# Kernel tuning notes

Measured on AMD Instinct MI355X. Metric: run time of the kernel, lower is better.

Reference implementation:

```python
import jax, jax.numpy as jnp
import numpy as np
from jax import lax

# Mamba2 block (training path: mamba_split_conv1d_scan_combined equivalent)
B = 2; L = 2048; D_MODEL = 2048
INTER = 4096          # ssm_intermediate_size
NH = 64; HD = INTER // NH   # num_heads, head_dim
N = 128               # ssm_state_size
G = 1                 # n_groups
K = 4                 # conv kernel
CS = 256              # chunk size
EPS = 1e-5
CONV_DIM = INTER + 2 * G * N          # 4352
PROJ_DIM = INTER + CONV_DIM + NH      # 8512


def setup_inputs() -> dict:
    key = jax.random.key(0)
    ks = jax.random.split(key, 4)
    std = 0.02
    return {
        "hidden_states": jax.random.normal(ks[0], (B, L, D_MODEL), jnp.float32),
        "W_in": jax.random.normal(ks[1], (PROJ_DIM, D_MODEL), jnp.float32) * std,
        "conv_w": jax.random.normal(ks[2], (CONV_DIM, K), jnp.float32) * std,
        "conv_b": jnp.zeros((CONV_DIM,), jnp.float32),
        "dt_bias": jnp.ones((NH,), jnp.float32),
        "A_log": jnp.log(jnp.arange(1, NH + 1, dtype=jnp.float32)),
        "D": jnp.ones((NH,), jnp.float32),
        "norm_w": jnp.ones((INTER,), jnp.float32),
        "W_out": jax.random.normal(ks[3], (D_MODEL, INTER), jnp.float32) * std,
    }


def _segsum(x):
    # x: [..., s] -> [..., s, s] lower-triangular cumulative sums (masked with -inf)
    s = x.shape[-1]
    xc = jnp.cumsum(x, axis=-1)
    d = xc[..., :, None] - xc[..., None, :]
    return jnp.where(jnp.tril(jnp.ones((s, s), dtype=bool)), d, -jnp.inf)


def _forward(hidden_states, W_in, conv_w, conv_b, dt_bias, A_log, D, norm_w, W_out):
    proj = hidden_states @ W_in.T                              # [B,L,PROJ_DIM]
    gate = proj[..., :INTER]
    hBC = proj[..., INTER:INTER + CONV_DIM]
    dt = proj[..., INTER + CONV_DIM:]                          # [B,L,NH]

    # causal depthwise conv1d + silu
    xc = hBC.transpose(0, 2, 1)                                # [B,CONV_DIM,L]
    y = lax.conv_general_dilated(
        xc, conv_w[:, None, :], (1,), [(K - 1, 0)],
        dimension_numbers=("NCH", "OIH", "NCH"), feature_group_count=CONV_DIM)
    hBC = jax.nn.silu(y + conv_b[None, :, None]).transpose(0, 2, 1)

    x = hBC[..., :INTER].reshape(B, L, NH, HD)
    Bm = hBC[..., INTER:INTER + G * N].reshape(B, L, G, N)
    Cm = hBC[..., INTER + G * N:].reshape(B, L, G, N)

    dtv = jax.nn.softplus(dt + dt_bias)                        # [B,L,NH], dt_softplus=True
    A = -jnp.exp(A_log)                                        # [NH]

    # ---- chunked selective scan (SSD) ----
    c = L // CS
    xch = x.reshape(B, c, CS, NH, HD)
    dtch = dtv.reshape(B, c, CS, NH)
    Bh = jnp.repeat(Bm.reshape(B, c, CS, G, N), NH // G, axis=3)   # [B,c,s,NH,N]
    Ch = jnp.repeat(Cm.reshape(B, c, CS, G, N), NH // G, axis=3)

    dA = (dtch * A).transpose(0, 3, 1, 2)                      # [B,NH,c,s]
    Acum = jnp.cumsum(dA, axis=-1)                             # [B,NH,c,s]
    Lmat = jnp.exp(_segsum(dA))                                # [B,NH,c,s,s]

    # within-chunk (diagonal block) output
    Ydiag = jnp.einsum("bcihn,bcjhn,bhcij,bcjh,bcjhp->bcihp",
                       Ch, Bh, Lmat, dtch, xch)

    # per-chunk states
    decay_states = jnp.exp(Acum[..., -1:] - Acum)              # [B,NH,c,s]
    states = jnp.einsum("bcjhn,bhcj,bcjh,bcjhp->bchpn",
                        Bh, decay_states, dtch, xch)           # [B,c,NH,HD,N]

    # inter-chunk recurrence (scan over chunks)
    chunk_decay = jnp.exp(Acum[..., -1])                       # [B,NH,c]

    def step(carry, inp):
        st, dec = inp
        new = dec[:, :, None, None] * carry + st
        return new, carry                                      # emit state at chunk start

    init = jnp.zeros((B, NH, HD, N), dtype=x.dtype)
    _, prev = lax.scan(step, init,
                       (states.transpose(1, 0, 2, 3, 4), chunk_decay.transpose(2, 0, 1)))
    prev = prev.transpose(1, 0, 2, 3, 4)                       # [B,c,NH,HD,N]

    Yoff = jnp.einsum("bcihn,bchpn,bhci->bcihp", Ch, prev, jnp.exp(Acum))

    Y = (Ydiag + Yoff).reshape(B, L, NH, HD) + x * D[None, None, :, None]
    yout = Y.reshape(B, L, INTER)

    # gated RMSNorm (norm_before_gate=False): gate first, then normalize
    yout = yout * jax.nn.silu(gate)
    yout = yout * lax.rsqrt(jnp.mean(yout * yout, axis=-1, keepdims=True) + EPS) * norm_w
    return yout @ W_out.T                                      # [B,L,D_MODEL]


def reference(hidden_states, W_in, conv_w, conv_b, dt_bias, A_log, D, norm_w, W_out):
    return _forward(hidden_states, W_in, conv_w, conv_b, dt_bias, A_log, D, norm_w, W_out)
```

## Files before the change

kernel.cpp:

```cpp
#include <hip/hip_runtime.h>
#include <cstdint>

typedef __bf16 bf16;
typedef __bf16 bf16x8 __attribute__((ext_vector_type(8)));
typedef __bf16 bf16x4 __attribute__((ext_vector_type(4)));
typedef float  f32x4  __attribute__((ext_vector_type(4)));

#define BQ     2
#define LQ     2048
#define DMODEL 2048
#define INTER  4096
#define NH     64
#define HD     64
#define NS     128
#define CS     256
#define NC     8
#define CONVD  4352
#define PROJD  8512
#define PROJP  8576
#define MTOT   4096
#define EPSF   1e-5f
#define LOG2E  1.44269504088896f

__device__ __forceinline__ void async_ld16(const bf16* g, bf16* l) {
  __builtin_amdgcn_global_load_lds(
      (__attribute__((address_space(1))) void*)(uintptr_t)g,
      (__attribute__((address_space(3))) void*)l, 16, 0, 0);
}

__device__ __forceinline__ float siluf(float x) { return x / (1.f + expf(-x)); }

__global__ void cast4_k(const float* __restrict__ in, bf16* __restrict__ out, long n4) {
  long i = (long)blockIdx.x * 256 + threadIdx.x;
  if (i >= n4) return;
  float4 v = ((const float4*)in)[i];
  bf16x4 o; o[0] = (bf16)v.x; o[1] = (bf16)v.y; o[2] = (bf16)v.z; o[3] = (bf16)v.w;
  ((bf16x4*)out)[i] = o;
}

__global__ void cast_pad_win_k(const float* __restrict__ W, bf16* __restrict__ out) {
  long i = (long)blockIdx.x * 256 + threadIdx.x;
  long tot = (long)PROJP * (DMODEL / 4);
  if (i >= tot) return;
  long row = i / (DMODEL / 4);
  long k4  = i % (DMODEL / 4);
  bf16x4 o;
  if (row < PROJD) {
    float4 v = ((const float4*)W)[row * (DMODEL / 4) + k4];
    o[0] = (bf16)v.x; o[1] = (bf16)v.y; o[2] = (bf16)v.z; o[3] = (bf16)v.w;
  } else {
    o[0] = o[1] = o[2] = o[3] = (bf16)0.f;
  }
  ((bf16x4*)out)[i] = o;
}

#define BM 128
#define BN 128
#define BK 64

__global__ __launch_bounds__(256) void gemm_bt(
    const bf16* __restrict__ A, const bf16* __restrict__ W,
    bf16* __restrict__ Cb, float* __restrict__ Cf,
    int M, int Nn, int K, int outf32)
{
  __shared__ bf16 As[BM * BK];
  __shared__ bf16 Bs[BN * BK];
  const int tid  = threadIdx.x;
  const int wave = tid >> 6;
  const int lane = tid & 63;

  int bxi, byi;
  {
    int b = blockIdx.y * gridDim.x + blockIdx.x;
    if ((gridDim.y & 7) == 0) {
      int gs = gridDim.x * 8;
      int g = b / gs, r = b % gs;
      byi = g * 8 + (r & 7);
      bxi = r >> 3;
    } else { bxi = blockIdx.x; byi = blockIdx.y; }
  }
  const long tm = (long)byi * BM;
  const long tn = (long)bxi * BN;
  const int wm = (wave >> 1) * 64;
  const int wn = (wave & 1) * 64;
  const int quad = lane >> 4;
  const int r16  = lane & 15;

  const int srow = wave * 8 + (lane >> 3);
  const int scg  = (lane & 7) ^ (lane >> 3);

  f32x4 acc[4][4] = {};

  for (long k0 = 0; k0 < K; k0 += BK) {
    __syncthreads();
    #pragma unroll
    for (int p = 0; p < 4; ++p) {
      const bf16* ga = A + (tm + p * 32 + srow) * K + k0 + scg * 8;
      const bf16* gw = W + (tn + p * 32 + srow) * K + k0 + scg * 8;
      async_ld16(ga, &As[p * 2048 + wave * 512]);
      async_ld16(gw, &Bs[p * 2048 + wave * 512]);
    }
    __syncthreads();
    #pragma unroll
    for (int ks = 0; ks < 2; ++ks) {
      bf16x8 af[4], bfr[4];
      #pragma unroll
      for (int i = 0; i < 4; ++i) {
        int r = wm + i * 16 + r16;
        int slot = (ks * 4 + quad) ^ (r & 7);
        af[i] = *(const bf16x8*)&As[r * 64 + slot * 8];
      }
      #pragma unroll
      for (int j = 0; j < 4; ++j) {
        int r = wn + j * 16 + r16;
        int slot = (ks * 4 + quad) ^ (r & 7);
        bfr[j] = *(const bf16x8*)&Bs[r * 64 + slot * 8];
      }
      #pragma unroll
      for (int i = 0; i < 4; ++i)
        #pragma unroll
        for (int j = 0; j < 4; ++j)
          acc[i][j] = __builtin_amdgcn_mfma_f32_16x16x32_bf16(af[i], bfr[j], acc[i][j], 0, 0, 0);
    }
  }

  #pragma unroll
  for (int i = 0; i < 4; ++i)
    #pragma unroll
    for (int j = 0; j < 4; ++j) {
      long r0 = tm + wm + i * 16 + quad * 4;
      long cc = tn + wn + j * 16 + r16;
      #pragma unroll
      for (int reg = 0; reg < 4; ++reg) {
        long idx = (r0 + reg) * (long)Nn + cc;
        if (outf32) Cf[idx] = acc[i][j][reg];
        else        Cb[idx] = (bf16)acc[i][j][reg];
      }
    }
}

__global__ void conv_silu_k(const bf16* __restrict__ proj,
                            const float* __restrict__ conv_w,
                            const float* __restrict__ conv_b,
                            bf16* __restrict__ xconv,
                            bf16* __restrict__ Bmb, bf16* __restrict__ Cmb,
                            bf16* __restrict__ Bt)
{
  int ch = blockIdx.x * 256 + threadIdx.x;
  if (ch >= CONVD) return;
  long bl = blockIdx.y;
  int l = (int)(bl & (LQ - 1));
  float acc = conv_b[ch];
  #pragma unroll
  for (int t = 0; t < 4; ++t) {
    int ls = l - 3 + t;
    if (ls >= 0)
      acc += (float)proj[(bl - 3 + t) * PROJP + INTER + ch] * conv_w[ch * 4 + t];
  }
  float y = siluf(acc);
  if (ch < INTER) {
    xconv[bl * INTER + ch] = (bf16)y;
  } else if (ch < INTER + NS) {
    int n = ch - INTER;
    Bmb[bl * NS + n] = (bf16)y;
    int b = (int)(bl >> 11), ci = l >> 8, j = l & 255;
    Bt[(((long)(b * NC + ci) * NS) + n) * CS + j] = (bf16)y;
  } else {
    Cmb[bl * NS + (ch - INTER - NS)] = (bf16)y;
  }
}

__global__ __launch_bounds__(CS) void dt_prep_k(
    const bf16* __restrict__ proj, const float* __restrict__ dt_bias,
    const float* __restrict__ A_log,
    float* __restrict__ dtv, float* __restrict__ acum, float* __restrict__ cdec)
{
  int bx = blockIdx.x;
  int ci = bx & 7;
  int bh = bx >> 3;
  int h  = bh & 63;
  int b  = bh >> 6;
  int i  = threadIdx.x;
  long pos = (long)b * LQ + ci * CS + i;
  float draw = (float)proj[pos * PROJP + INTER + CONVD + h] + dt_bias[h];
  float dv = draw > 20.f ? draw : log1pf(expf(draw));
  float Ah = -expf(A_log[h]);
  __shared__ float s[CS];
  s[i] = dv * Ah;
  __syncthreads();
  for (int off = 1; off < CS; off <<= 1) {
    float t = (i >= off) ? s[i - off] : 0.f;
    __syncthreads();
    s[i] += t;
    __syncthreads();
  }
  long base = (long)bx * CS;
  dtv[base + i]  = dv;
  acum[base + i] = s[i];
  if (i == 0) cdec[bx] = expf(s[CS - 1]);
}

__global__ __launch_bounds__(256) void gmat_k(
    const bf16* __restrict__ Cmb, const bf16* __restrict__ Bmb, float* __restrict__ Gnt)
{
  int q  = blockIdx.x;
  int bc = blockIdx.y;
  long bl0 = (long)(bc >> 3) * LQ + (bc & 7) * CS;
  int wave = threadIdx.x >> 6, lane = threadIdx.x & 63;
  int quad = lane >> 4, r16 = lane & 15;
  int i0 = (q >> 1) * 128 + (wave >> 1) * 64;
  int j0 = (q & 1)  * 128 + (wave & 1)  * 64;

  f32x4 acc[4][4] = {};
  #pragma unroll
  for (int kt = 0; kt < 4; ++kt) {
    int k0 = kt * 32 + quad * 8;
    bf16x8 af[4], bfv[4];
    #pragma unroll
    for (int it = 0; it < 4; ++it)
      af[it] = *(const bf16x8*)&Cmb[(bl0 + i0 + it * 16 + r16) * NS + k0];
    #pragma unroll
    for (int nt = 0; nt < 4; ++nt)
      bfv[nt] = *(const bf16x8*)&Bmb[(bl0 + j0 + nt * 16 + r16) * NS + k0];
    #pragma unroll
    for (int it = 0; it < 4; ++it)
      #pragma unroll
      for (int nt = 0; nt < 4; ++nt)
        acc[it][nt] = __builtin_amdgcn_mfma_f32_16x16x32_bf16(af[it], bfv[nt], acc[it][nt], 0, 0, 0);
  }
  #pragma unroll
  for (int it = 0; it < 4; ++it)
    #pragma unroll
    for (int nt = 0; nt < 4; ++nt)
      #pragma unroll
      for (int reg = 0; reg < 4; ++reg) {
        int i = i0 + it * 16 + quad * 4 + reg;
        int j = j0 + nt * 16 + r16;
        Gnt[((long)bc * CS + i) * CS + j] = acc[it][nt][reg];
      }
}

__global__ __launch_bounds__(256) void states_k(
    const bf16* __restrict__ xconv, const bf16* __restrict__ Bt,
    const float* __restrict__ dtv, const float* __restrict__ acum,
    bf16* __restrict__ st)
{
  int bx = blockIdx.x;
  int h = bx & 63, bc = bx >> 6;
  int b = bc >> 3, ci = bc & 7;
  long bl0 = (long)b * LQ + ci * CS;
  long abase = ((long)(b * NH + h) * NC + ci) * CS;
  int t = threadIdx.x;
  int wave = t >> 6, lane = t & 63, quad = lane >> 4, r16 = lane & 15;

  __shared__ bf16 Xt[64][264];
  __shared__ float ws[CS];
  __shared__ float ac_s[CS];
  ac_s[t] = acum[abase + t];
  __syncthreads();
  float alast = ac_s[CS - 1];
  ws[t] = expf(alast - ac_s[t]) * dtv[abase + t];
  {
    int col = t & 63, grp = t >> 6;
    for (int r = 0; r < 64; ++r) {
      int j = grp * 64 + r;
      Xt[col][j] = xconv[(bl0 + j) * INTER + h * HD + col];
    }
  }
  __syncthreads();

  const bf16* btb = &Bt[(long)bc * NS * CS];
  f32x4 acc[8] = {};
  int p = wave * 16 + r16;
  #pragma unroll
  for (int kt = 0; kt < 8; ++kt) {
    int k0 = kt * 32 + quad * 8;
    bf16x8 xv = *(const bf16x8*)&Xt[p][k0];
    float w8[8];
    *(float4*)&w8[0] = *(const float4*)&ws[k0];
    *(float4*)&w8[4] = *(const float4*)&ws[k0 + 4];
    bf16x8 af;
    #pragma unroll
    for (int jj = 0; jj < 8; ++jj) af[jj] = (bf16)((float)xv[jj] * w8[jj]);
    #pragma unroll
    for (int nt = 0; nt < 8; ++nt) {
      bf16x8 bfv = *(const bf16x8*)&btb[(nt * 16 + r16) * CS + k0];
      acc[nt] = __builtin_amdgcn_mfma_f32_16x16x32_bf16(af, bfv, acc[nt], 0, 0, 0);
    }
  }
  #pragma unroll
  for (int nt = 0; nt < 8; ++nt)
    #pragma unroll
    for (int reg = 0; reg < 4; ++reg) {
      int prow = wave * 16 + quad * 4 + reg;
      int n = nt * 16 + r16;
      st[((long)bx * HD + prow) * NS + n] = (bf16)acc[nt][reg];
    }
}

__global__ void scan_k(bf16* __restrict__ st, const float* __restrict__ cdec)
{
  long t = (long)blockIdx.x * 256 + threadIdx.x;
  int n = (int)(t & 127);
  int p = (int)((t >> 7) & 63);
  int h = (int)((t >> 13) & 63);
  int b = (int)(t >> 19);
  float carry = 0.f;
  for (int ci = 0; ci < NC; ++ci) {
    long idx = (((long)(b * NC + ci) * NH + h) * HD + p) * NS + n;
    float v = (float)st[idx];
    st[idx] = (bf16)carry;
    carry = cdec[(b * NH + h) * NC + ci] * carry + v;
  }
}

#define XTP 392
__global__ __launch_bounds__(256) void ymix_k(
    const bf16* __restrict__ xconv, const float* __restrict__ Gnt,
    const bf16* __restrict__ prev, const bf16* __restrict__ Cmb,
    const float* __restrict__ dtv, const float* __restrict__ acum,
    const float* __restrict__ Dp, bf16* __restrict__ Y)
{
  int bx = blockIdx.x;
  int h = bx & 63, bc = bx >> 6;
  int b = bc >> 3, ci = bc & 7;
  long bl0 = (long)b * LQ + ci * CS;
  long abase = ((long)(b * NH + h) * NC + ci) * CS;
  int t = threadIdx.x;
  int wave = t >> 6, lane = t & 63;
  int quad = lane >> 4, r16 = lane & 15;
  int iw = wave * 64;

  __shared__ bf16 Xt[64][XTP];
  __shared__ float a2s[CS], dts[CS], eas[CS];

  {
    float ac = acum[abase + t];
    a2s[t] = ac * LOG2E;
    dts[t] = dtv[abase + t];
    eas[t] = expf(ac);
  }
  {
    int col = t & 63, grp = t >> 6;
    for (int r = 0; r < 64; ++r) {
      int j = grp * 64 + r;
      Xt[col][j] = xconv[(bl0 + j) * INTER + h * HD + col];
    }
  }
  for (int r = 0; r < 32; ++r) {
    int idx = t + r * 256;
    int n = idx & 127, p = idx >> 7;
    Xt[p][256 + n] = prev[((long)bx * HD + p) * NS + n];
  }
  __syncthreads();

  f32x4 acc[4][4] = {};

  for (int kt = 0; kt < 12; ++kt) {
    int k0 = kt * 32;
    bool cpart = (k0 >= 256);
    if (!cpart && k0 > iw + 63) continue;

    bf16x8 bfrag[4];
    #pragma unroll
    for (int nt = 0; nt < 4; ++nt)
      bfrag[nt] = *(const bf16x8*)&Xt[nt * 16 + r16][k0 + quad * 8];

    if (!cpart) {
      int j0 = k0 + quad * 8;
      float dt8[8], a28[8];
      *(float4*)&dt8[0] = *(const float4*)&dts[j0];
      *(float4*)&dt8[4] = *(const float4*)&dts[j0 + 4];
      *(float4*)&a28[0] = *(const float4*)&a2s[j0];
      *(float4*)&a28[4] = *(const float4*)&a2s[j0 + 4];
      #pragma unroll
      for (int it = 0; it < 4; ++it) {
        if (k0 > iw + it * 16 + 15) continue;
        int i = iw + it * 16 + r16;
        float a2i = a2s[i];
        const float* gp = &Gnt[((long)bc * CS + i) * CS + j0];
        float g[8];
        *(float4*)&g[0] = *(const float4*)gp;
        *(float4*)&g[4] = *(const float4*)(gp + 4);
        bf16x8 af;
        #pragma unroll
        for (int jj = 0; jj < 8; ++jj) {
          float v = g[jj] * dt8[jj] * exp2f(a2i - a28[jj]);
          v = (j0 + jj <= i) ? v : 0.f;
          af[jj] = (bf16)v;
        }
        #pragma unroll
        for (int nt = 0; nt < 4; ++nt)
          acc[it][nt] = __builtin_amdgcn_mfma_f32_16x16x32_bf16(af, bfrag[nt], acc[it][nt], 0, 0, 0);
      }
    } else {
      int n0 = k0 - 256 + quad * 8;
      #pragma unroll
      for (int it = 0; it < 4; ++it) {
        int i = iw + it * 16 + r16;
        float e = eas[i];
        bf16x8 cv = *(const bf16x8*)&Cmb[(bl0 + i) * NS + n0];
        bf16x8 af;
        #pragma unroll
        for (int jj = 0; jj < 8; ++jj)
          af[jj] = (bf16)(e * (float)cv[jj]);
        #pragma unroll
        for (int nt = 0; nt < 4; ++nt)
          acc[it][nt] = __builtin_amdgcn_mfma_f32_16x16x32_bf16(af, bfrag[nt], acc[it][nt], 0, 0, 0);
      }
    }
  }

  float Dh = Dp[h];
  #pragma unroll
  for (int it = 0; it < 4; ++it)
    #pragma unroll
    for (int nt = 0; nt < 4; ++nt) {
      int i0 = iw + it * 16 + quad * 4;
      int p  = nt * 16 + r16;
      bf16x4 xv = *(const bf16x4*)&Xt[p][i0];
      #pragma unroll
      for (int reg = 0; reg < 4; ++reg) {
        float v = acc[it][nt][reg] + Dh * (float)xv[reg];
        Y[(bl0 + i0 + reg) * INTER + h * HD + p] = (bf16)v;
      }
    }
}

__global__ __launch_bounds__(256) void norm_k(
    bf16* __restrict__ Y, const bf16* __restrict__ proj,
    const float* __restrict__ norm_w)
{
  long bl = blockIdx.x;
  int t = threadIdx.x;
  __shared__ float yb[INTER];
  __shared__ float red[256];
  float ss = 0.f;
  for (int r = 0; r < 16; ++r) {
    int ch = t + r * 256;
    float g = (float)proj[bl * PROJP + ch];
    float yv = (float)Y[bl * INTER + ch] * siluf(g);
    yb[ch] = yv;
    ss += yv * yv;
  }
  red[t] = ss;
  __syncthreads();
  for (int s = 128; s > 0; s >>= 1) {
    if (t < s) red[t] += red[t + s];
    __syncthreads();
  }
  float scale = rsqrtf(red[0] / (float)INTER + EPSF);
  for (int r = 0; r < 16; ++r) {
    int ch = t + r * 256;
    Y[bl * INTER + ch] = (bf16)(yb[ch] * scale * norm_w[ch]);
  }
}

extern "C" void kernel_launch(void* const* d_in, const int* in_sizes, int n_in,
                              void* d_out, int out_size, void* d_ws, size_t ws_size,
                              hipStream_t stream)
{
  (void)in_sizes; (void)n_in; (void)out_size; (void)ws_size;
  const float* hidden  = (const float*)d_in[0];
  const float* W_in    = (const float*)d_in[1];
  const float* conv_w  = (const float*)d_in[2];
  const float* conv_b  = (const float*)d_in[3];
  const float* dt_bias = (const float*)d_in[4];
  const float* A_log   = (const float*)d_in[5];
  const float* Dp      = (const float*)d_in[6];
  const float* norm_w  = (const float*)d_in[7];
  const float* W_out   = (const float*)d_in[8];
  float* out = (float*)d_out;

  char* ws    = (char*)d_ws;
  bf16* projb = (bf16*)(ws);
  char* base2 = ws + 70254592;
  bf16*  hb    = (bf16*)(base2);
  bf16*  winb  = (bf16*)(base2 + 16777216);
  bf16*  xconv = (bf16*)(base2);
  bf16*  st    = (bf16*)(base2 + 33554432);
  float* Gnt   = (float*)(base2 + 50331648);
  bf16*  Bmb   = (bf16*)(base2 + 54525952);
  bf16*  Cmb   = (bf16*)(base2 + 55574528);
  float* dtv   = (float*)(base2 + 56623104);
  float* acum  = (float*)(base2 + 57671680);
  float* cdec  = (float*)(base2 + 58720256);
  bf16*  Bt    = (bf16*)(base2 + 58724352);
  bf16*  Yb    = xconv;
  bf16*  woutb = st;

  cast4_k<<<dim3((unsigned)((MTOT * (long)DMODEL / 4 + 255) / 256)), 256, 0, stream>>>(
      hidden, hb, (long)MTOT * DMODEL / 4);
  cast_pad_win_k<<<dim3((unsigned)(((long)PROJP * (DMODEL / 4) + 255) / 256)), 256, 0, stream>>>(
      W_in, winb);
  gemm_bt<<<dim3(PROJP / BN, MTOT / BM), 256, 0, stream>>>(
      hb, winb, projb, nullptr, MTOT, PROJP, DMODEL, 0);

  conv_silu_k<<<dim3(CONVD / 256, MTOT), 256, 0, stream>>>(
      projb, conv_w, conv_b, xconv, Bmb, Cmb, Bt);
  dt_prep_k<<<dim3(BQ * NH * NC), CS, 0, stream>>>(
      projb, dt_bias, A_log, dtv, acum, cdec);
  gmat_k<<<dim3(4, BQ * NC), 256, 0, stream>>>(Cmb, Bmb, Gnt);
  states_k<<<dim3(BQ * NC * NH), 256, 0, stream>>>(xconv, Bt, dtv, acum, st);
  scan_k<<<dim3(BQ * NH * HD * NS / 256), 256, 0, stream>>>(st, cdec);
  ymix_k<<<dim3(BQ * NC * NH), 256, 0, stream>>>(
      xconv, Gnt, st, Cmb, dtv, acum, Dp, Yb);

  cast4_k<<<dim3((unsigned)((DMODEL * (long)INTER / 4 + 255) / 256)), 256, 0, stream>>>(
      W_out, woutb, (long)DMODEL * INTER / 4);
  norm_k<<<dim3(MTOT), 256, 0, stream>>>(Yb, projb, norm_w);
  gemm_bt<<<dim3(DMODEL / BN, MTOT / BM), 256, 0, stream>>>(
      Yb, woutb, nullptr, out, MTOT, DMODEL, INTER, 1);
}
```

Baseline: 706.0 us.

## Replace GEMM with 256x256 pipelined 8-wave kernel and split-K out-projection

Replaces the 128x128 single-buffered bf16 GEMM with a 256x256-tile, 512-thread kernel. It double-buffers LDS via async global-to-LDS loads and interleaves staging with MFMA phases under explicit barriers and priority hints. The output projection uses split-K=2 into fp32 partials in the workspace, followed by a reduction kernel, so more workgroups are available. W_in padding grows to a multiple of 256 rows. The cost is an extra reduction pass and extra partial traffic, plus fragile hand-written waitcnt scheduling.

```diff
diff --git a/kernel.cpp b/kernel.cpp
--- a/kernel.cpp
+++ b/kernel.cpp
@@ -18,6 +18,7 @@
 #define CONVD  4352
 #define PROJD  8512
 #define PROJP  8576
+#define PROJW  8704
 #define MTOT   4096
 #define EPSF   1e-5f
 #define LOG2E  1.44269504088896f
@@ -29,6 +30,10 @@
 }
 
 __device__ __forceinline__ float siluf(float x) { return x / (1.f + expf(-x)); }
+
+#define SB()    __builtin_amdgcn_sched_barrier(0)
+#define HWBAR() __builtin_amdgcn_s_barrier()
+#define LGKM0() asm volatile("s_waitcnt lgkmcnt(0)" ::: "memory")
 
 __global__ void cast4_k(const float* __restrict__ in, bf16* __restrict__ out, long n4) {
   long i = (long)blockIdx.x * 256 + threadIdx.x;
@@ -40,7 +45,7 @@
 
 __global__ void cast_pad_win_k(const float* __restrict__ W, bf16* __restrict__ out) {
   long i = (long)blockIdx.x * 256 + threadIdx.x;
-  long tot = (long)PROJP * (DMODEL / 4);
+  long tot = (long)PROJW * (DMODEL / 4);
   if (i >= tot) return;
   long row = i / (DMODEL / 4);
   long k4  = i % (DMODEL / 4);
@@ -54,89 +59,151 @@
   ((bf16x4*)out)[i] = o;
 }
 
-#define BM 128
-#define BN 128
-#define BK 64
-
-__global__ __launch_bounds__(256) void gemm_bt(
+
+template<int R0>
+__device__ __forceinline__ void ldfrag(bf16x8 (&dst)[4][2], const char* base,
+                                       int r16, int quad, int xr) {
+  #pragma unroll
+  for (int f = 0; f < 4; ++f)
+    #pragma unroll
+    for (int kk = 0; kk < 2; ++kk)
+      dst[f][kk] = *(const bf16x8*)(base + (((R0 + f) * 16 + r16) << 7)
+                                         + ((((kk << 2) + quad) ^ xr) << 4));
+}
+
+template<int M0, int I0>
+__device__ __forceinline__ void qmfma(f32x4 (&acc)[8][4], const bf16x8 (&ar)[4][2],
+                                      const bf16x8 (&b)[4][2]) {
+  #pragma unroll
+  for (int mm = 0; mm < 2; ++mm)
+    #pragma unroll
+    for (int nf = 0; nf < 4; ++nf)
+      #pragma unroll
+      for (int kk = 0; kk < 2; ++kk)
+        acc[M0 + mm][nf] = __builtin_amdgcn_mfma_f32_16x16x32_bf16(
+            ar[I0 + mm][kk], b[nf][kk], acc[M0 + mm][nf], 0, 0, 0);
+}
+
+__global__ __launch_bounds__(512, 2) void gemm8(
     const bf16* __restrict__ A, const bf16* __restrict__ W,
     bf16* __restrict__ Cb, float* __restrict__ Cf,
-    int M, int Nn, int K, int outf32)
-{
-  __shared__ bf16 As[BM * BK];
-  __shared__ bf16 Bs[BN * BK];
+    int M, int Nn, int Ntiles, int K, int KS, int outf32)
+{
+  __shared__ int4 lds4[8192];
+  char* lds = (char*)lds4;
   const int tid  = threadIdx.x;
-  const int wave = tid >> 6;
-  const int lane = tid & 63;
-
-  int bxi, byi;
-  {
-    int b = blockIdx.y * gridDim.x + blockIdx.x;
-    if ((gridDim.y & 7) == 0) {
-      int gs = gridDim.x * 8;
-      int g = b / gs, r = b % gs;
-      byi = g * 8 + (r & 7);
-      bxi = r >> 3;
-    } else { bxi = blockIdx.x; byi = blockIdx.y; }
-  }
-  const long tm = (long)byi * BM;
-  const long tn = (long)bxi * BN;
-  const int wm = (wave >> 1) * 64;
-  const int wn = (wave & 1) * 64;
-  const int quad = lane >> 4;
-  const int r16  = lane & 15;
-
-  const int srow = wave * 8 + (lane >> 3);
-  const int scg  = (lane & 7) ^ (lane >> 3);
-
-  f32x4 acc[4][4] = {};
-
-  for (long k0 = 0; k0 < K; k0 += BK) {
-    __syncthreads();
-    #pragma unroll
-    for (int p = 0; p < 4; ++p) {
-      const bf16* ga = A + (tm + p * 32 + srow) * K + k0 + scg * 8;
-      const bf16* gw = W + (tn + p * 32 + srow) * K + k0 + scg * 8;
-      async_ld16(ga, &As[p * 2048 + wave * 512]);
-      async_ld16(gw, &Bs[p * 2048 + wave * 512]);
-    }
-    __syncthreads();
-    #pragma unroll
-    for (int ks = 0; ks < 2; ++ks) {
-      bf16x8 af[4], bfr[4];
-      #pragma unroll
-      for (int i = 0; i < 4; ++i) {
-        int r = wm + i * 16 + r16;
-        int slot = (ks * 4 + quad) ^ (r & 7);
-        af[i] = *(const bf16x8*)&As[r * 64 + slot * 8];
+  const int w    = tid >> 6;
+  const int l    = tid & 63;
+  const int wm   = w >> 2;
+  const int wn   = w & 3;
+  const int quad = l >> 4;
+  const int r16  = l & 15;
+  const int xr   = r16 & 7;
+
+  const int Mtiles  = M >> 8;
+  const int tilesMN = Mtiles * Ntiles;
+  const int nwg = tilesMN * KS;
+  int bid = blockIdx.x;
+  int sid = ((nwg & 7) == 0) ? ((bid & 7) * (nwg >> 3) + (bid >> 3)) : bid;
+  const int ks  = sid / tilesMN;
+  const int rem = sid - ks * tilesMN;
+  const int by = rem % Mtiles;
+  const int bx = rem / Mtiles;
+  const long tm = (long)by << 8;
+  const long tn = (long)bx << 8;
+  const int  NT = K / (64 * KS);
+  const long kbase = (long)ks * (K / KS);
+
+  const int srow = w * 8 + (l >> 3);
+  const int scg  = (l & 7) ^ ((l >> 3) & 7);
+  const bf16* Ab = A + (tm + srow) * K + kbase + scg * 8;
+  const bf16* Wb = W + (tn + srow) * K + kbase + scg * 8;
+
+  auto stage = [&](int tile, int part) {
+    if (tile < NT) {
+      const bf16* s = (part < 2 ? Ab : Wb) + (long)((part & 1) * 128) * K + (long)tile * 64;
+      char* d = lds + ((tile & 1) << 16) + (part << 14) + (w << 10);
+      async_ld16(s, (bf16*)d);
+      async_ld16(s + (long)K * 64, (bf16*)(d + 8192));
+    }
+  };
+
+  stage(0, 0); stage(0, 1); stage(0, 2); stage(0, 3);
+  stage(1, 2); stage(1, 0); stage(1, 1);
+  SB();
+  asm volatile("s_waitcnt vmcnt(6)" ::: "memory");
+  SB();
+  HWBAR();
+  SB();
+
+  f32x4 acc[8][4] = {};
+
+  for (int T = 0; T < NT; ++T) {
+    const int bsel = (T & 1) << 16;
+    const char* as = lds + bsel + (wm << 14);
+    const char* bs = lds + bsel + 32768 + ((wn >> 1) << 14) + ((wn & 1) << 13);
+    bf16x8 a0[4][2], a1[4][2], b[4][2];
+
+    ldfrag<0>(b,  bs, r16, quad, xr);
+    ldfrag<0>(a0, as, r16, quad, xr);
+    stage(T + 1, 3);
+    SB(); HWBAR(); LGKM0(); SB();
+    __builtin_amdgcn_s_setprio(1);
+    qmfma<0, 0>(acc, a0, b);
+    __builtin_amdgcn_s_setprio(0);
+    SB(); HWBAR(); SB();
+
+    ldfrag<4>(a1, as, r16, quad, xr);
+    stage(T + 2, 2);
+    SB(); HWBAR(); LGKM0(); SB();
+    __builtin_amdgcn_s_setprio(1);
+    qmfma<2, 2>(acc, a0, b);
+    __builtin_amdgcn_s_setprio(0);
+    SB(); HWBAR(); SB();
+
+    stage(T + 2, 0);
+    SB(); HWBAR(); LGKM0(); SB();
+    __builtin_amdgcn_s_setprio(1);
+    qmfma<4, 0>(acc, a1, b);
+    __builtin_amdgcn_s_setprio(0);
+    SB(); HWBAR(); SB();
+
+    stage(T + 2, 1);
+    SB(); HWBAR(); LGKM0(); SB();
+    __builtin_amdgcn_s_setprio(1);
+    qmfma<6, 2>(acc, a1, b);
+    __builtin_amdgcn_s_setprio(0);
+    SB();
+    if (T + 2 < NT) { asm volatile("s_waitcnt vmcnt(6)" ::: "memory"); }
+    else            { asm volatile("s_waitcnt vmcnt(0)" ::: "memory"); }
+    SB(); HWBAR(); SB();
+  }
+
+  const long cbase = (long)ks * M * Nn;
+  #pragma unroll
+  for (int mf = 0; mf < 8; ++mf)
+    #pragma unroll
+    for (int nf = 0; nf < 4; ++nf) {
+      long r0 = tm + wm * 128 + mf * 16 + quad * 4;
+      long cc = tn + wn * 64 + nf * 16 + r16;
+      if (cc < Nn) {
+        #pragma unroll
+        for (int reg = 0; reg < 4; ++reg) {
+          long idx = (r0 + reg) * (long)Nn + cc;
+          if (outf32) Cf[cbase + idx] = acc[mf][nf][reg];
+          else        Cb[idx] = (bf16)acc[mf][nf][reg];
+        }
       }
-      #pragma unroll
-      for (int j = 0; j < 4; ++j) {
-        int r = wn + j * 16 + r16;
-        int slot = (ks * 4 + quad) ^ (r & 7);
-        bfr[j] = *(const bf16x8*)&Bs[r * 64 + slot * 8];
-      }
-      #pragma unroll
-      for (int i = 0; i < 4; ++i)
-        #pragma unroll
-        for (int j = 0; j < 4; ++j)
-          acc[i][j] = __builtin_amdgcn_mfma_f32_16x16x32_bf16(af[i], bfr[j], acc[i][j], 0, 0, 0);
-    }
-  }
-
-  #pragma unroll
-  for (int i = 0; i < 4; ++i)
-    #pragma unroll
-    for (int j = 0; j < 4; ++j) {
-      long r0 = tm + wm + i * 16 + quad * 4;
-      long cc = tn + wn + j * 16 + r16;
-      #pragma unroll
-      for (int reg = 0; reg < 4; ++reg) {
-        long idx = (r0 + reg) * (long)Nn + cc;
-        if (outf32) Cf[idx] = acc[i][j][reg];
-        else        Cb[idx] = (bf16)acc[i][j][reg];
-      }
-    }
+    }
+}
+
+__global__ void addred_k(const float* __restrict__ P, float* __restrict__ out, long n4) {
+  long i = (long)blockIdx.x * 256 + threadIdx.x;
+  if (i >= n4) return;
+  float4 a = ((const float4*)P)[i];
+  float4 b = ((const float4*)P)[i + n4];
+  float4 r; r.x = a.x + b.x; r.y = a.y + b.y; r.z = a.z + b.z; r.w = a.w + b.w;
+  ((float4*)out)[i] = r;
 }
 
 __global__ void conv_silu_k(const bf16* __restrict__ proj,
@@ -491,10 +558,10 @@
 
   cast4_k<<<dim3((unsigned)((MTOT * (long)DMODEL / 4 + 255) / 256)), 256, 0, stream>>>(
       hidden, hb, (long)MTOT * DMODEL / 4);
-  cast_pad_win_k<<<dim3((unsigned)(((long)PROJP * (DMODEL / 4) + 255) / 256)), 256, 0, stream>>>(
+  cast_pad_win_k<<<dim3((unsigned)(((long)PROJW * (DMODEL / 4) + 255) / 256)), 256, 0, stream>>>(
       W_in, winb);
-  gemm_bt<<<dim3(PROJP / BN, MTOT / BM), 256, 0, stream>>>(
-      hb, winb, projb, nullptr, MTOT, PROJP, DMODEL, 0);
+  gemm8<<<dim3((PROJW / 256) * (MTOT / 256)), 512, 0, stream>>>(
+      hb, winb, projb, nullptr, MTOT, PROJP, PROJW / 256, DMODEL, 1, 0);
 
   conv_silu_k<<<dim3(CONVD / 256, MTOT), 256, 0, stream>>>(
       projb, conv_w, conv_b, xconv, Bmb, Cmb, Bt);
@@ -509,6 +576,8 @@
   cast4_k<<<dim3((unsigned)((DMODEL * (long)INTER / 4 + 255) / 256)), 256, 0, stream>>>(
       W_out, woutb, (long)DMODEL * INTER / 4);
   norm_k<<<dim3(MTOT), 256, 0, stream>>>(Yb, projb, norm_w);
-  gemm_bt<<<dim3(DMODEL / BN, MTOT / BM), 256, 0, stream>>>(
-      Yb, woutb, nullptr, out, MTOT, DMODEL, INTER, 1);
-}
+  gemm8<<<dim3((DMODEL / 256) * (MTOT / 256) * 2), 512, 0, stream>>>(
+      Yb, woutb, nullptr, (float*)projb, MTOT, DMODEL, DMODEL / 256, INTER, 2, 1);
+  addred_k<<<dim3((unsigned)((MTOT * (long)DMODEL / 4 + 255) / 256)), 256, 0, stream>>>(
+      (const float*)projb, out, (long)MTOT * DMODEL / 4);
+}
```

New measurement: 663.7 us. 6.0% less time.
